# Optimization experiments

Hardware: AMD Instinct MI355X
Metric: run time of the kernel (lower is better)

Reference implementation:

```python
import jax, jax.numpy as jnp
import numpy as np

N = 50000      # nodes
E = 800000     # edges (before self-loops)
H = 2          # attention heads
C = 64         # hidden_channels (per-head out since concat=False)
L = 3          # num_layers - 2 conv blocks
OUT = 128      # readout out_channels
G = 512        # num graphs
VOCAB = 100    # embedding table size
NEG_SLOPE = 0.2


def setup_inputs() -> dict:
    key = jax.random.key(0)
    ks = jax.random.split(key, 12)
    s = 1.0 / np.sqrt(C)
    x = jax.random.randint(ks[0], (N,), 0, VOCAB, dtype=jnp.int32)
    edge_index = jax.random.randint(ks[1], (2, E), 0, N, dtype=jnp.int32)
    batch = jnp.sort(jax.random.randint(ks[2], (N,), 0, G, dtype=jnp.int32))
    embed = jax.random.normal(ks[3], (VOCAB, C), dtype=jnp.float32) * s
    lin_W = jax.random.normal(ks[4], (L, C, C), dtype=jnp.float32) * s
    lin_b = jnp.zeros((L, C), dtype=jnp.float32)
    gat_Wl = jax.random.normal(ks[5], (L, C, H * C), dtype=jnp.float32) * s
    gat_bl = jnp.zeros((L, H * C), dtype=jnp.float32)
    gat_Wr = jax.random.normal(ks[6], (L, C, H * C), dtype=jnp.float32) * s
    gat_br = jnp.zeros((L, H * C), dtype=jnp.float32)
    gat_att = jax.random.normal(ks[7], (L, H, C), dtype=jnp.float32) * s
    gat_bias = jnp.zeros((L, C), dtype=jnp.float32)
    readout_W = jax.random.normal(ks[8], (C, OUT), dtype=jnp.float32) * s
    readout_b = jnp.zeros((OUT,), dtype=jnp.float32)
    return {"x": x, "edge_index": edge_index, "batch": batch, "num_graphs": G,
            "embed": embed, "lin_W": lin_W, "lin_b": lin_b,
            "gat_Wl": gat_Wl, "gat_bl": gat_bl, "gat_Wr": gat_Wr, "gat_br": gat_br,
            "gat_att": gat_att, "gat_bias": gat_bias,
            "readout_W": readout_W, "readout_b": readout_b}


def _gatv2_layer(h, src, dst, Wl, bl, Wr, br, att, bias):
    # lin_l -> source/message features, lin_r -> target features (PyG GATv2Conv)
    xl = (h @ Wl + bl).reshape(N, H, C)
    xr = (h @ Wr + br).reshape(N, H, C)
    # per-edge GATv2 score: a^T LeakyReLU(x_l[j] + x_r[i])
    e = jax.nn.leaky_relu(xl[src] + xr[dst], NEG_SLOPE)      # [E2,H,C]
    score = jnp.einsum('ehc,hc->eh', e, att)                 # [E2,H]
    # segment softmax over incoming edges of each dst node (stable)
    m = jax.lax.stop_gradient(jax.ops.segment_max(score, dst, num_segments=N))
    p = jnp.exp(score - m[dst])
    denom = jax.ops.segment_sum(p, dst, num_segments=N)      # [N,H]
    alpha = p / denom[dst]                                   # [E2,H]
    msg = xl[src] * alpha[:, :, None]                        # [E2,H,C]
    agg = jax.ops.segment_sum(msg, dst, num_segments=N)      # [N,H,C]
    return agg.mean(axis=1) + bias                           # concat=False -> head mean


def reference(x, edge_index, batch, num_graphs, embed, lin_W, lin_b,
              gat_Wl, gat_bl, gat_Wr, gat_br, gat_att, gat_bias,
              readout_W, readout_b):
    # add self loops (GATv2Conv default add_self_loops=True)
    loops = jnp.arange(N, dtype=edge_index.dtype)
    src = jnp.concatenate([edge_index[0], loops])
    dst = jnp.concatenate([edge_index[1], loops])
    h = embed[x]                                             # [N,C]
    for l in range(L):
        h = jax.nn.relu(h @ lin_W[l] + lin_b[l])             # dropout is a no-op in eval
        h = _gatv2_layer(h, src, dst, gat_Wl[l], gat_bl[l], gat_Wr[l], gat_br[l],
                         gat_att[l], gat_bias[l])
    out = h @ readout_W + readout_b                          # [N,OUT]
    return jax.ops.segment_sum(out, batch, num_segments=num_graphs)  # [G,OUT]
```

## Files before the change

kernel.cpp:

```cpp
#include <hip/hip_runtime.h>
#include <hip/hip_fp16.h>

#define N_NODES  50000
#define E_EDGES  800000
#define E_TOT    850000
#define H_HEADS  2
#define C_DIM    64
#define HC       128
#define L_LAYERS 3
#define OUT_DIM  128
#define G_GRAPHS 512
#define NEG_SLOPE 0.2f
#define SCAN_B   196
#define NB       196
#define EPB      4096

typedef float v2f __attribute__((ext_vector_type(2)));

__device__ __forceinline__ void lds_fence() { asm volatile("" ::: "memory"); }

__global__ void embed_kernel(const int* __restrict__ x, const float* __restrict__ embed,
                             float* __restrict__ h, int* __restrict__ counts) {
    int i = blockIdx.x * 256 + threadIdx.x;
    if (i < N_NODES) counts[i] = 0;
    if (i >= N_NODES * C_DIM) return;
    int n = i >> 6, c = i & 63;
    h[i] = embed[x[n] * C_DIM + c];
}

__global__ void csr_count_kernel(const int* __restrict__ dsts, int* __restrict__ counts) {
    int e = blockIdx.x * 256 + threadIdx.x;
    if (e >= E_TOT) return;
    int d = (e < E_EDGES) ? dsts[e] : e - E_EDGES;
    atomicAdd(&counts[d], 1);
}

__global__ void scan_partial_kernel(const int* __restrict__ counts, int* __restrict__ row_ptr,
                                    int* __restrict__ partials) {
    __shared__ int wsum[4];
    int i = blockIdx.x * 256 + threadIdx.x;
    int lane = threadIdx.x & 63, wid = threadIdx.x >> 6;
    int cnt = (i < N_NODES) ? counts[i] : 0;
    int v = cnt;
#pragma unroll
    for (int off = 1; off < 64; off <<= 1) {
        int t = __shfl_up(v, off, 64);
        if (lane >= off) v += t;
    }
    if (lane == 63) wsum[wid] = v;
    __syncthreads();
    int woff = 0;
#pragma unroll
    for (int w = 0; w < 4; w++) if (w < wid) woff += wsum[w];
    v += woff;
    if (i < N_NODES) row_ptr[i] = v - cnt;
    if (threadIdx.x == 255) partials[blockIdx.x] = v;
}

__global__ void scan_offsets_kernel(const int* __restrict__ partials, int* __restrict__ block_off) {
    __shared__ int wsum[4];
    int tid = threadIdx.x;
    int lane = tid & 63, wid = tid >> 6;
    int cnt = (tid < SCAN_B) ? partials[tid] : 0;
    int v = cnt;
#pragma unroll
    for (int off = 1; off < 64; off <<= 1) {
        int t = __shfl_up(v, off, 64);
        if (lane >= off) v += t;
    }
    if (lane == 63) wsum[wid] = v;
    __syncthreads();
    int woff = 0;
#pragma unroll
    for (int w = 0; w < 4; w++) if (w < wid) woff += wsum[w];
    v += woff;
    if (tid < SCAN_B) block_off[tid] = v - cnt;
}

__global__ void scan_add_kernel(int* __restrict__ row_ptr, const int* __restrict__ block_off,
                                int* __restrict__ bwptr) {
    int i = blockIdx.x * 256 + threadIdx.x;
    if (i < N_NODES) {
        int v = row_ptr[i] + block_off[blockIdx.x];
        row_ptr[i] = v;
        if ((i & 255) == 0) bwptr[i >> 8] = v;
    }
    if (i == 0) row_ptr[N_NODES] = E_TOT;
}

__global__ void edge_partition_kernel(const int* __restrict__ srcs, const int* __restrict__ dsts,
                                      int* __restrict__ bwptr, unsigned int* __restrict__ ebuf) {
    __shared__ int hist[256];
    __shared__ int lscan[256];
    __shared__ int sExcl[256];
    __shared__ int lcnt[256];
    __shared__ int gbase[256];
    __shared__ unsigned int sval[EPB];
    __shared__ unsigned char sgid[EPB];
    int tid = threadIdx.x;
    int ebase = blockIdx.x * EPB;
    hist[tid] = 0;
    __syncthreads();
    unsigned int val[16];
    int gid[16];
#pragma unroll
    for (int i = 0; i < 16; i++) {
        int e = ebase + i * 256 + tid;
        if (e < E_TOT) {
            int s, d;
            if (e < E_EDGES) { s = srcs[e]; d = dsts[e]; }
            else             { s = d = e - E_EDGES; }
            val[i] = ((unsigned)s << 8) | (unsigned)(d & 255);
            gid[i] = d >> 8;
            atomicAdd(&hist[gid[i]], 1);
        } else gid[i] = -1;
    }
    __syncthreads();
    lscan[tid] = hist[tid];
    __syncthreads();
#pragma unroll
    for (int off = 1; off < 256; off <<= 1) {
        int t = (tid >= off) ? lscan[tid - off] : 0;
        __syncthreads();
        lscan[tid] += t;
        __syncthreads();
    }
    sExcl[tid] = lscan[tid] - hist[tid];
    lcnt[tid] = 0;
    __syncthreads();
#pragma unroll
    for (int i = 0; i < 16; i++) {
        if (gid[i] >= 0) {
            int off = atomicAdd(&lcnt[gid[i]], 1);
            int idx = sExcl[gid[i]] + off;
            sval[idx] = val[i];
            sgid[idx] = (unsigned char)gid[i];
        }
    }
    if (tid < NB) {
        int c = hist[tid];
        gbase[tid] = c ? atomicAdd(&bwptr[tid], c) : 0;
    }
    __syncthreads();
    int total = lscan[255];
    for (int idx = tid; idx < total; idx += 256) {
        int g = sgid[idx];
        ebuf[gbase[g] + (idx - sExcl[g])] = sval[idx];
    }
}

__global__ void bucket_csr_kernel(const unsigned int* __restrict__ ebuf,
                                  const int* __restrict__ row_ptr,
                                  unsigned short* __restrict__ src_sorted) {
    __shared__ int lbase[256];
    __shared__ int lcnt[256];
    int g = blockIdx.x, tid = threadIdx.x;
    int n0 = g << 8;
    int nodes = min(256, N_NODES - n0);
    int b0 = row_ptr[n0];
    int b1 = row_ptr[min(n0 + 256, N_NODES)];
    if (tid < nodes) lbase[tid] = row_ptr[n0 + tid] - b0;
    lcnt[tid] = 0;
    __syncthreads();
    int cnt = b1 - b0;
    for (int i = tid; i < cnt; i += 256) {
        unsigned int v = ebuf[b0 + i];
        int dl = v & 255;
        int slot = lbase[dl] + atomicAdd(&lcnt[dl], 1);
        src_sorted[b0 + slot] = (unsigned short)(v >> 8);
    }
}

__global__ void layer_lin_kernel(const float* __restrict__ h,
                                 const float* __restrict__ W, const float* __restrict__ b,
                                 const float* __restrict__ Wl, const float* __restrict__ bl,
                                 const float* __restrict__ Wr, const float* __restrict__ br,
                                 __half* __restrict__ xlh, float* __restrict__ xri) {
    __shared__ float sH[16 * 64];
    __shared__ float sH2[16 * 64];
    int tid = threadIdx.x;
    int base = blockIdx.x * 16;
#pragma unroll
    for (int i = 0; i < 4; i++) {
        int idx = tid + i * 256;
        int nn = base + (idx >> 6);
        sH[idx] = (nn < N_NODES) ? h[(size_t)nn * 64 + (idx & 63)] : 0.f;
    }
    __syncthreads();
    {
        int c = tid & 63, g = tid >> 6;
        float a0 = b[c], a1 = a0, a2 = a0, a3 = a0;
        for (int k = 0; k < 64; k++) {
            float wv = W[k * 64 + c];
            a0 = fmaf(sH[(g * 4 + 0) * 64 + k], wv, a0);
            a1 = fmaf(sH[(g * 4 + 1) * 64 + k], wv, a1);
            a2 = fmaf(sH[(g * 4 + 2) * 64 + k], wv, a2);
            a3 = fmaf(sH[(g * 4 + 3) * 64 + k], wv, a3);
        }
        sH2[(g * 4 + 0) * 64 + c] = fmaxf(a0, 0.f);
        sH2[(g * 4 + 1) * 64 + c] = fmaxf(a1, 0.f);
        sH2[(g * 4 + 2) * 64 + c] = fmaxf(a2, 0.f);
        sH2[(g * 4 + 3) * 64 + c] = fmaxf(a3, 0.f);
    }
    __syncthreads();
    {
        int j = tid & 127, gg = tid >> 7;
        float accl[8], accr[8];
#pragma unroll
        for (int n = 0; n < 8; n++) { accl[n] = bl[j]; accr[n] = br[j]; }
        for (int k = 0; k < 64; k++) {
            float wl = Wl[k * 128 + j], wr = Wr[k * 128 + j];
#pragma unroll
            for (int n = 0; n < 8; n++) {
                float hv = sH2[(gg * 8 + n) * 64 + k];
                accl[n] = fmaf(hv, wl, accl[n]);
                accr[n] = fmaf(hv, wr, accr[n]);
            }
        }
        int hh = j >> 6, c = j & 63;
#pragma unroll
        for (int n = 0; n < 8; n++) {
            int node = base + gg * 8 + n;
            if (node < N_NODES) {
                size_t o = (size_t)node * 128 + c * 2 + hh;
                xlh[o] = __float2half(accl[n]);
                xri[o] = accr[n];
            }
        }
    }
}

__global__ void gat_kernel(const __half2* __restrict__ xlh, const float2* __restrict__ xr2,
                           const float* __restrict__ att, const int* __restrict__ row_ptr,
                           const unsigned short* __restrict__ src_sorted,
                           const float* __restrict__ bias,
                           float* __restrict__ h_out) {
    __shared__ __align__(16) float cbuf[4][8 * 132];
    int w = threadIdx.x >> 6;
    int d = blockIdx.x * 4 + w;
    if (d >= N_NODES) return;
    int lane = threadIdx.x & 63;
    int r0 = row_ptr[d], r1 = row_ptr[d + 1];
    float2 vrf = xr2[(size_t)d * 64 + lane];
    v2f vr2 = {vrf.x, vrf.y};
    v2f att2 = {att[lane], att[64 + lane]};
    float* cb = cbuf[w];
    int e_of = lane >> 3, p = lane & 7;

    float dpx = 0.f, dpy = 0.f;
    v2f ac0 = {0.f, 0.f}, ac1 = {0.f, 0.f};

#define GAT_LOAD(V, CB) do {                                                    \
        int lim_ = nchunk - 1;                                                  \
        _Pragma("unroll")                                                       \
        for (int e = 0; e < 8; e++) {                                           \
            int ee_ = (CB) + e;                                                 \
            int sv_ = __builtin_amdgcn_readlane(idx, (ee_ < nchunk) ? ee_ : lim_); \
            V[e] = xlh[(size_t)sv_ * 64 + lane];                                \
        }                                                                       \
    } while (0)

#define GAT_PROC(V, CB) do {                                                    \
        int rem_ = nchunk - (CB);                                               \
        v2f vf8[8];                                                             \
        _Pragma("unroll")                                                       \
        for (int e = 0; e < 8; e++) {                                           \
            float2 vf_ = __half22float2(V[e]);                                  \
            v2f vl2 = {vf_.x, vf_.y};                                           \
            vf8[e] = vl2;                                                       \
            v2f z = vl2 + vr2;                                                  \
            v2f t = __builtin_elementwise_max(z, z * NEG_SLOPE) * att2;         \
            *(v2f*)&cb[e * 132 + 2 * lane] = t;                                 \
        }                                                                       \
        lds_fence();                                                            \
        v2f s2 = {0.f, 0.f};                                                    \
        {                                                                       \
            const float4* row_ = (const float4*)&cb[e_of * 132 + p * 16];       \
            _Pragma("unroll")                                                   \
            for (int j = 0; j < 4; j++) {                                       \
                float4 f = row_[j];                                             \
                s2 += (v2f){f.x, f.y};                                          \
                s2 += (v2f){f.z, f.w};                                          \
            }                                                                   \
        }                                                                       \
        lds_fence();                                                            \
        _Pragma("unroll")                                                       \
        for (int off = 1; off <= 4; off <<= 1) {                                \
            v2f o_;                                                             \
            o_.x = __shfl_xor(s2.x, off, 64);                                   \
            o_.y = __shfl_xor(s2.y, off, 64);                                   \
            s2 += o_;                                                           \
        }                                                                       \
        float sx = s2.x, sy = s2.y;                                             \
        if (e_of >= rem_) { sx = -INFINITY; sy = -INFINITY; }                   \
        float wx = __expf(sx), wy = __expf(sy);                                 \
        dpx += wx; dpy += wy;                                                   \
        _Pragma("unroll")                                                       \
        for (int e = 0; e < 8; e++) {                                           \
            float swx = __int_as_float(__builtin_amdgcn_readlane(__float_as_int(wx), 8 * e)); \
            float swy = __int_as_float(__builtin_amdgcn_readlane(__float_as_int(wy), 8 * e)); \
            v2f w2 = {swx, swy};                                                \
            if (e & 1) ac1 = __builtin_elementwise_fma(w2, vf8[e], ac1);        \
            else       ac0 = __builtin_elementwise_fma(w2, vf8[e], ac0);        \
        }                                                                       \
    } while (0)

    for (int base = r0; base < r1; base += 64) {
        int a = base + lane;
        int idx = (int)src_sorted[(a < r1) ? a : (r1 - 1)];
        int nchunk = min(64, r1 - base);
        __half2 va[8], vb[8];
        GAT_LOAD(va, 0);
        int cb_i = 0;
        for (;;) {
            int nx = cb_i + 8;
            if (nx < nchunk) {
                GAT_LOAD(vb, nx);
                GAT_PROC(va, cb_i);
                cb_i = nx;
            } else {
                GAT_PROC(va, cb_i);
                break;
            }
            nx = cb_i + 8;
            if (nx < nchunk) {
                GAT_LOAD(va, nx);
                GAT_PROC(vb, cb_i);
                cb_i = nx;
            } else {
                GAT_PROC(vb, cb_i);
                break;
            }
        }
    }
#undef GAT_LOAD
#undef GAT_PROC

#pragma unroll
    for (int off = 8; off <= 32; off <<= 1) {
        dpx += __shfl_xor(dpx, off, 64);
        dpy += __shfl_xor(dpy, off, 64);
    }
    v2f acc = ac0 + ac1;
    h_out[(size_t)d * 64 + lane] = (acc.x / dpx + acc.y / dpy) * 0.5f + bias[lane];
}

__global__ void zero_out_kernel(float* __restrict__ out) {
    int i = blockIdx.x * 256 + threadIdx.x;
    if (i < G_GRAPHS * OUT_DIM) out[i] = 0.f;
}

__global__ void readout_kernel(const float* __restrict__ h, const float* __restrict__ W,
                               const float* __restrict__ b, const int* __restrict__ batch,
                               float* __restrict__ out) {
    __shared__ float sH[16 * 64];
    __shared__ int sB[16];
    int tid = threadIdx.x;
    int base = blockIdx.x * 16;
#pragma unroll
    for (int i = 0; i < 4; i++) {
        int idx = tid + i * 256;
        int nn = base + (idx >> 6);
        sH[idx] = (nn < N_NODES) ? h[(size_t)nn * 64 + (idx & 63)] : 0.f;
    }
    if (tid < 16) sB[tid] = (base + tid < N_NODES) ? batch[base + tid] : -1;
    __syncthreads();
    int j = tid & 127, gg = tid >> 7;
    float acc[8];
#pragma unroll
    for (int n = 0; n < 8; n++) acc[n] = b[j];
    for (int k = 0; k < 64; k++) {
        float wv = W[k * OUT_DIM + j];
#pragma unroll
        for (int n = 0; n < 8; n++) acc[n] = fmaf(sH[(gg * 8 + n) * 64 + k], wv, acc[n]);
    }
    float run = 0.f; int curb = -2;
#pragma unroll
    for (int n = 0; n < 8; n++) {
        int node = base + gg * 8 + n;
        int bb = (node < N_NODES) ? sB[gg * 8 + n] : -1;
        if (bb != curb) {
            if (curb >= 0) atomicAdd(&out[curb * OUT_DIM + j], run);
            run = 0.f; curb = bb;
        }
        if (bb >= 0) run += acc[n];
    }
    if (curb >= 0) atomicAdd(&out[curb * OUT_DIM + j], run);
}

extern "C" void kernel_launch(void* const* d_in, const int* in_sizes, int n_in,
                              void* d_out, int out_size, void* d_ws, size_t ws_size,
                              hipStream_t stream) {
    const int*   x        = (const int*)d_in[0];
    const int*   edge     = (const int*)d_in[1];
    const int*   batch    = (const int*)d_in[2];
    const float* embed    = (const float*)d_in[4];
    const float* lin_W    = (const float*)d_in[5];
    const float* lin_b    = (const float*)d_in[6];
    const float* gat_Wl   = (const float*)d_in[7];
    const float* gat_bl   = (const float*)d_in[8];
    const float* gat_Wr   = (const float*)d_in[9];
    const float* gat_br   = (const float*)d_in[10];
    const float* gat_att  = (const float*)d_in[11];
    const float* gat_bias = (const float*)d_in[12];
    const float* ro_W     = (const float*)d_in[13];
    const float* ro_b     = (const float*)d_in[14];
    float* out = (float*)d_out;

    const int* srcs = edge;
    const int* dsts = edge + E_EDGES;

    float* h    = (float*)d_ws;
    __half* xlh = (__half*)(h + (size_t)N_NODES * 64);
    float* xr   = (float*)((char*)xlh + (size_t)N_NODES * HC * sizeof(__half));
    int* counts     = (int*)(xr + (size_t)N_NODES * HC);
    int* row_ptr    = counts + N_NODES;
    int* bwptr      = row_ptr + N_NODES + 1;
    int* partials   = bwptr + 256;
    int* block_off  = partials + SCAN_B;
    unsigned int* ebuf = (unsigned int*)(block_off + SCAN_B);
    unsigned short* src_sorted = (unsigned short*)(ebuf + E_TOT);

    const int T = 256;
    const int gEmbed = (N_NODES * C_DIM + 255) / 256;
    const int gEdge  = (E_TOT + 255) / 256;
    const int gPart  = (E_TOT + EPB - 1) / EPB;
    const int gLin   = (N_NODES + 15) / 16;
    const int gGat   = (N_NODES + 3) / 4;
    const int gOut   = (G_GRAPHS * OUT_DIM + 255) / 256;

    embed_kernel<<<gEmbed, T, 0, stream>>>(x, embed, h, counts);

    csr_count_kernel<<<gEdge, T, 0, stream>>>(dsts, counts);
    scan_partial_kernel<<<SCAN_B, T, 0, stream>>>(counts, row_ptr, partials);
    scan_offsets_kernel<<<1, T, 0, stream>>>(partials, block_off);
    scan_add_kernel<<<SCAN_B, T, 0, stream>>>(row_ptr, block_off, bwptr);
    edge_partition_kernel<<<gPart, T, 0, stream>>>(srcs, dsts, bwptr, ebuf);
    bucket_csr_kernel<<<NB, T, 0, stream>>>(ebuf, row_ptr, src_sorted);

    for (int l = 0; l < L_LAYERS; l++) {
        layer_lin_kernel<<<gLin, T, 0, stream>>>(
            h,
            lin_W + (size_t)l * 64 * 64, lin_b + (size_t)l * 64,
            gat_Wl + (size_t)l * 64 * 128, gat_bl + (size_t)l * 128,
            gat_Wr + (size_t)l * 64 * 128, gat_br + (size_t)l * 128,
            xlh, xr);
        gat_kernel<<<gGat, T, 0, stream>>>(
            (const __half2*)xlh, (const float2*)xr, gat_att + (size_t)l * HC,
            row_ptr, src_sorted, gat_bias + (size_t)l * 64, h);
    }

    zero_out_kernel<<<gOut, T, 0, stream>>>(out);
    readout_kernel<<<gLin, T, 0, stream>>>(h, ro_W, ro_b, batch, out);
}
```

Before: 451.9 us.

## Build CSR via bucket-level counts and fuse embedding gather into first linear layer

Replaces the per-node atomic degree count and three-kernel scan with a per-bucket (256-node) histogram in shared memory and a single 196-entry scan. Each bucket's CSR row pointers are then derived locally inside bucket_csr_kernel from a per-bucket histogram and block scan. The embedding lookup moves into the first layer_lin_kernel, and output zeroing is folded into the init kernel. Together these remove several launches and a full pass over 850k global atomics, in exchange for an extra histogram pass over ebuf inside the bucket kernel.

After: 407.8 us. -9.7%, faster.

```diff
diff --git a/kernel.cpp b/kernel.cpp
--- a/kernel.cpp
+++ b/kernel.cpp
@@ -11,7 +11,6 @@
 #define OUT_DIM  128
 #define G_GRAPHS 512
 #define NEG_SLOPE 0.2f
-#define SCAN_B   196
 #define NB       196
 #define EPB      4096
 
@@ -19,28 +18,36 @@
 
 __device__ __forceinline__ void lds_fence() { asm volatile("" ::: "memory"); }
 
-__global__ void embed_kernel(const int* __restrict__ x, const float* __restrict__ embed,
-                             float* __restrict__ h, int* __restrict__ counts) {
+__global__ void init_kernel(float* __restrict__ out, int* __restrict__ bucket_counts) {
     int i = blockIdx.x * 256 + threadIdx.x;
-    if (i < N_NODES) counts[i] = 0;
-    if (i >= N_NODES * C_DIM) return;
-    int n = i >> 6, c = i & 63;
-    h[i] = embed[x[n] * C_DIM + c];
-}
-
-__global__ void csr_count_kernel(const int* __restrict__ dsts, int* __restrict__ counts) {
-    int e = blockIdx.x * 256 + threadIdx.x;
-    if (e >= E_TOT) return;
-    int d = (e < E_EDGES) ? dsts[e] : e - E_EDGES;
-    atomicAdd(&counts[d], 1);
-}
-
-__global__ void scan_partial_kernel(const int* __restrict__ counts, int* __restrict__ row_ptr,
-                                    int* __restrict__ partials) {
+    if (i < G_GRAPHS * OUT_DIM) out[i] = 0.f;
+    if (blockIdx.x == 0) bucket_counts[threadIdx.x] = 0;
+}
+
+__global__ void bucket_count_kernel(const int* __restrict__ dsts, int* __restrict__ bucket_counts) {
+    __shared__ int hist[256];
+    int tid = threadIdx.x;
+    hist[tid] = 0;
+    __syncthreads();
+    int ebase = blockIdx.x * EPB;
+#pragma unroll
+    for (int i = 0; i < 16; i++) {
+        int e = ebase + i * 256 + tid;
+        if (e < E_TOT) {
+            int d = (e < E_EDGES) ? dsts[e] : e - E_EDGES;
+            atomicAdd(&hist[d >> 8], 1);
+        }
+    }
+    __syncthreads();
+    if (hist[tid]) atomicAdd(&bucket_counts[tid], hist[tid]);
+}
+
+__global__ void scan196_kernel(const int* __restrict__ bucket_counts,
+                               int* __restrict__ bwptr, int* __restrict__ bbase) {
     __shared__ int wsum[4];
-    int i = blockIdx.x * 256 + threadIdx.x;
-    int lane = threadIdx.x & 63, wid = threadIdx.x >> 6;
-    int cnt = (i < N_NODES) ? counts[i] : 0;
+    int tid = threadIdx.x;
+    int lane = tid & 63, wid = tid >> 6;
+    int cnt = (tid < NB) ? bucket_counts[tid] : 0;
     int v = cnt;
 #pragma unroll
     for (int off = 1; off < 64; off <<= 1) {
@@ -53,39 +60,8 @@
 #pragma unroll
     for (int w = 0; w < 4; w++) if (w < wid) woff += wsum[w];
     v += woff;
-    if (i < N_NODES) row_ptr[i] = v - cnt;
-    if (threadIdx.x == 255) partials[blockIdx.x] = v;
-}
-
-__global__ void scan_offsets_kernel(const int* __restrict__ partials, int* __restrict__ block_off) {
-    __shared__ int wsum[4];
-    int tid = threadIdx.x;
-    int lane = tid & 63, wid = tid >> 6;
-    int cnt = (tid < SCAN_B) ? partials[tid] : 0;
-    int v = cnt;
-#pragma unroll
-    for (int off = 1; off < 64; off <<= 1) {
-        int t = __shfl_up(v, off, 64);
-        if (lane >= off) v += t;
-    }
-    if (lane == 63) wsum[wid] = v;
-    __syncthreads();
-    int woff = 0;
-#pragma unroll
-    for (int w = 0; w < 4; w++) if (w < wid) woff += wsum[w];
-    v += woff;
-    if (tid < SCAN_B) block_off[tid] = v - cnt;
-}
-
-__global__ void scan_add_kernel(int* __restrict__ row_ptr, const int* __restrict__ block_off,
-                                int* __restrict__ bwptr) {
-    int i = blockIdx.x * 256 + threadIdx.x;
-    if (i < N_NODES) {
-        int v = row_ptr[i] + block_off[blockIdx.x];
-        row_ptr[i] = v;
-        if ((i & 255) == 0) bwptr[i >> 8] = v;
-    }
-    if (i == 0) row_ptr[N_NODES] = E_TOT;
+    if (tid < NB) { bwptr[tid] = v - cnt; bbase[tid] = v - cnt; }
+    if (tid == 0) bbase[NB] = E_TOT;
 }
 
 __global__ void edge_partition_kernel(const int* __restrict__ srcs, const int* __restrict__ dsts,
@@ -150,28 +126,53 @@
 }
 
 __global__ void bucket_csr_kernel(const unsigned int* __restrict__ ebuf,
-                                  const int* __restrict__ row_ptr,
+                                  const int* __restrict__ bbase,
+                                  int* __restrict__ row_ptr,
                                   unsigned short* __restrict__ src_sorted) {
-    __shared__ int lbase[256];
+    __shared__ int hist[256];
     __shared__ int lcnt[256];
+    __shared__ int wsum[4];
     int g = blockIdx.x, tid = threadIdx.x;
     int n0 = g << 8;
     int nodes = min(256, N_NODES - n0);
-    int b0 = row_ptr[n0];
-    int b1 = row_ptr[min(n0 + 256, N_NODES)];
-    if (tid < nodes) lbase[tid] = row_ptr[n0 + tid] - b0;
+    int b0 = bbase[g], b1 = bbase[g + 1];
+    int cnt = b1 - b0;
+    hist[tid] = 0;
     lcnt[tid] = 0;
     __syncthreads();
-    int cnt = b1 - b0;
+    for (int i = tid; i < cnt; i += 256) atomicAdd(&hist[ebuf[b0 + i] & 255], 1);
+    __syncthreads();
+    int c = hist[tid];
+    int v = c;
+    int lane = tid & 63, wid = tid >> 6;
+#pragma unroll
+    for (int off = 1; off < 64; off <<= 1) {
+        int t = __shfl_up(v, off, 64);
+        if (lane >= off) v += t;
+    }
+    if (lane == 63) wsum[wid] = v;
+    __syncthreads();
+    int woff = 0;
+#pragma unroll
+    for (int w = 0; w < 4; w++) if (w < wid) woff += wsum[w];
+    v += woff;
+    int nbase = b0 + v - c;
+    if (tid < nodes) row_ptr[n0 + tid] = nbase;
+    if (g == NB - 1 && tid == 0) row_ptr[N_NODES] = E_TOT;
+    __syncthreads();
+    hist[tid] = nbase;
+    __syncthreads();
     for (int i = tid; i < cnt; i += 256) {
-        unsigned int v = ebuf[b0 + i];
-        int dl = v & 255;
-        int slot = lbase[dl] + atomicAdd(&lcnt[dl], 1);
-        src_sorted[b0 + slot] = (unsigned short)(v >> 8);
+        unsigned int e = ebuf[b0 + i];
+        int dl = e & 255;
+        int slot = hist[dl] + atomicAdd(&lcnt[dl], 1);
+        src_sorted[slot] = (unsigned short)(e >> 8);
     }
 }
 
 __global__ void layer_lin_kernel(const float* __restrict__ h,
+                                 const int* __restrict__ xs, const float* __restrict__ etab,
+                                 int use_embed,
                                  const float* __restrict__ W, const float* __restrict__ b,
                                  const float* __restrict__ Wl, const float* __restrict__ bl,
                                  const float* __restrict__ Wr, const float* __restrict__ br,
@@ -184,7 +185,11 @@
     for (int i = 0; i < 4; i++) {
         int idx = tid + i * 256;
         int nn = base + (idx >> 6);
-        sH[idx] = (nn < N_NODES) ? h[(size_t)nn * 64 + (idx & 63)] : 0.f;
+        int cc = idx & 63;
+        float hv = 0.f;
+        if (nn < N_NODES)
+            hv = use_embed ? etab[xs[nn] * 64 + cc] : h[(size_t)nn * 64 + cc];
+        sH[idx] = hv;
     }
     __syncthreads();
     {
@@ -345,11 +350,6 @@
     h_out[(size_t)d * 64 + lane] = (acc.x / dpx + acc.y / dpy) * 0.5f + bias[lane];
 }
 
-__global__ void zero_out_kernel(float* __restrict__ out) {
-    int i = blockIdx.x * 256 + threadIdx.x;
-    if (i < G_GRAPHS * OUT_DIM) out[i] = 0.f;
-}
-
 __global__ void readout_kernel(const float* __restrict__ h, const float* __restrict__ W,
                                const float* __restrict__ b, const int* __restrict__ batch,
                                float* __restrict__ out) {
@@ -413,34 +413,28 @@
     float* h    = (float*)d_ws;
     __half* xlh = (__half*)(h + (size_t)N_NODES * 64);
     float* xr   = (float*)((char*)xlh + (size_t)N_NODES * HC * sizeof(__half));
-    int* counts     = (int*)(xr + (size_t)N_NODES * HC);
-    int* row_ptr    = counts + N_NODES;
-    int* bwptr      = row_ptr + N_NODES + 1;
-    int* partials   = bwptr + 256;
-    int* block_off  = partials + SCAN_B;
-    unsigned int* ebuf = (unsigned int*)(block_off + SCAN_B);
+    int* row_ptr       = (int*)(xr + (size_t)N_NODES * HC);
+    int* bwptr         = row_ptr + N_NODES + 1;
+    int* bbase         = bwptr + 256;
+    int* bucket_counts = bbase + 256;
+    unsigned int* ebuf = (unsigned int*)(bucket_counts + 256);
     unsigned short* src_sorted = (unsigned short*)(ebuf + E_TOT);
 
     const int T = 256;
-    const int gEmbed = (N_NODES * C_DIM + 255) / 256;
-    const int gEdge  = (E_TOT + 255) / 256;
-    const int gPart  = (E_TOT + EPB - 1) / EPB;
-    const int gLin   = (N_NODES + 15) / 16;
-    const int gGat   = (N_NODES + 3) / 4;
-    const int gOut   = (G_GRAPHS * OUT_DIM + 255) / 256;
-
-    embed_kernel<<<gEmbed, T, 0, stream>>>(x, embed, h, counts);
-
-    csr_count_kernel<<<gEdge, T, 0, stream>>>(dsts, counts);
-    scan_partial_kernel<<<SCAN_B, T, 0, stream>>>(counts, row_ptr, partials);
-    scan_offsets_kernel<<<1, T, 0, stream>>>(partials, block_off);
-    scan_add_kernel<<<SCAN_B, T, 0, stream>>>(row_ptr, block_off, bwptr);
+    const int gInit = (G_GRAPHS * OUT_DIM + 255) / 256;
+    const int gPart = (E_TOT + EPB - 1) / EPB;
+    const int gLin  = (N_NODES + 15) / 16;
+    const int gGat  = (N_NODES + 3) / 4;
+
+    init_kernel<<<gInit, T, 0, stream>>>(out, bucket_counts);
+    bucket_count_kernel<<<gPart, T, 0, stream>>>(dsts, bucket_counts);
+    scan196_kernel<<<1, T, 0, stream>>>(bucket_counts, bwptr, bbase);
     edge_partition_kernel<<<gPart, T, 0, stream>>>(srcs, dsts, bwptr, ebuf);
-    bucket_csr_kernel<<<NB, T, 0, stream>>>(ebuf, row_ptr, src_sorted);
+    bucket_csr_kernel<<<NB, T, 0, stream>>>(ebuf, bbase, row_ptr, src_sorted);
 
     for (int l = 0; l < L_LAYERS; l++) {
         layer_lin_kernel<<<gLin, T, 0, stream>>>(
-            h,
+            h, x, embed, (l == 0) ? 1 : 0,
             lin_W + (size_t)l * 64 * 64, lin_b + (size_t)l * 64,
             gat_Wl + (size_t)l * 64 * 128, gat_bl + (size_t)l * 128,
             gat_Wr + (size_t)l * 64 * 128, gat_br + (size_t)l * 128,
@@ -450,6 +444,5 @@
             row_ptr, src_sorted, gat_bias + (size_t)l * 64, h);
     }
 
-    zero_out_kernel<<<gOut, T, 0, stream>>>(out);
     readout_kernel<<<gLin, T, 0, stream>>>(h, ro_W, ro_b, batch, out);
 }
```
